# Kernel tuning notes

Measured on AMD Instinct MI355X. Metric: run time of the kernel, lower is better.

The kernel has to match this reference:

```python
import jax, jax.numpy as jnp
import numpy as np

NEG = -1e9

def setup_inputs() -> dict:
    key = jax.random.key(0)
    ks = jax.random.split(key, 8)
    B, Lc, Lq, D = 64, 1024, 128, 128
    C = jax.random.normal(ks[0], (B, Lc, D), dtype=jnp.float32)
    Q = jax.random.normal(ks[1], (B, Lq, D), dtype=jnp.float32)
    Cmask = jax.random.randint(ks[2], (B, Lc), 0, 2, dtype=jnp.int32)
    Qmask = jax.random.randint(ks[3], (B, Lq), 0, 2, dtype=jnp.int32)
    w_c = jax.random.normal(ks[4], (D, 1), dtype=jnp.float32) * (6.0 / (D + 1)) ** 0.5
    w_q = jax.random.normal(ks[5], (D, 1), dtype=jnp.float32) * (6.0 / (D + 1)) ** 0.5
    w_mul = jax.random.normal(ks[6], (1, 1, D), dtype=jnp.float32) * (6.0 / (D + 1)) ** 0.5
    bias = jnp.zeros((1,), dtype=jnp.float32)
    return {"C": C, "Q": Q, "Cmask": Cmask, "Qmask": Qmask,
            "w_c": w_c, "w_q": w_q, "w_mul": w_mul, "bias": bias}

def reference(C, Q, Cmask, Qmask, w_c, w_q, w_mul, bias):
    # Optimized trilinear similarity: S[b,i,j] = C.w_c + Q.w_q + (C*w_mul).Q^T + bias
    s0 = jnp.matmul(C, w_c)                        # [B,Lc,1]
    s1 = jnp.swapaxes(jnp.matmul(Q, w_q), 1, 2)    # [B,1,Lq]
    s2 = jnp.einsum('bid,bjd->bij', C * w_mul, Q)  # [B,Lc,Lq]
    S = s0 + s1 + s2 + bias
    qmask = (Qmask[:, None, :] == 0)               # [B,1,Lq]
    cmask = (Cmask[:, :, None] == 0)               # [B,Lc,1]
    S1 = jax.nn.softmax(jnp.where(qmask, NEG, S), axis=2)
    S2 = jax.nn.softmax(jnp.where(cmask, NEG, S), axis=1)
    A = jnp.matmul(S1, Q)                                       # [B,Lc,D]
    Bm = jnp.matmul(jnp.matmul(S1, jnp.swapaxes(S2, 1, 2)), C)  # [B,Lc,D]
    return jnp.concatenate([C, A, C * A, C * Bm], axis=2)
```

## Files before the change

### kernel.cpp

```cpp
#include <hip/hip_runtime.h>
#include <math.h>

constexpr int Bn = 64, Lc = 1024, Lq = 128, Dd = 128;

typedef __attribute__((ext_vector_type(8))) short short8_t;
typedef __attribute__((ext_vector_type(4))) short short4_t;
typedef __attribute__((ext_vector_type(4))) float f32x4;

__device__ __forceinline__ short f2bf(float x) {
    unsigned u = __float_as_uint(x);
    u += 0x7FFFu + ((u >> 16) & 1u);
    return (short)(u >> 16);
}

constexpr int AS = 132;
constexpr int TS = 70;
constexpr int CTS = 68;
constexpr int PS = 68;
constexpr int TBS = 36;

__device__ __forceinline__ void decode_bid(int n, int& b, int& blk) {
    b = (n & 7) * 8 + ((n >> 3) & 7);
    blk = n >> 6;
}

__global__ __launch_bounds__(256, 3) void k1_fused(
    const float* __restrict__ C, const float* __restrict__ Q,
    const int* __restrict__ Cmask, const int* __restrict__ Qmask,
    const float* __restrict__ w_c, const float* __restrict__ w_q,
    const float* __restrict__ w_mul, const float* __restrict__ bias,
    short* __restrict__ CT16,
    short* __restrict__ Q16, short* __restrict__ QT16,
    float* __restrict__ s0f, float* __restrict__ s1f,
    float* __restrict__ colpart, float* __restrict__ rowsumInv)
{
    __shared__ short Abuf[64 * AS];
    __shared__ short Bbuf[128 * AS];
    __shared__ float s0L[64], cmL[64], s1L[128], qmL[128];
    short* Tbuf = Bbuf;

    int b, blk; decode_bid(blockIdx.x, b, blk);
    int i0 = blk * 64, tid = threadIdx.x;

    const float4* C4 = (const float4*)(C + ((size_t)(b * Lc + i0)) * Dd);
    #pragma unroll
    for (int k = 0; k < 8; ++k) {
        int idx = tid + k * 256;
        int i = idx >> 5, d4 = idx & 31;
        float4 v = C4[idx];
        float4 wm = ((const float4*)w_mul)[d4];
        short4_t cw; cw[0]=f2bf(v.x*wm.x); cw[1]=f2bf(v.y*wm.y); cw[2]=f2bf(v.z*wm.z); cw[3]=f2bf(v.w*wm.w);
        *(short4_t*)&Abuf[i * AS + d4 * 4] = cw;
        float cm = (Cmask[b * Lc + i0 + i] != 0) ? 1.0f : 0.0f;
        Tbuf[(d4*4+0)*TS + i] = f2bf(cm * v.x);
        Tbuf[(d4*4+1)*TS + i] = f2bf(cm * v.y);
        Tbuf[(d4*4+2)*TS + i] = f2bf(cm * v.z);
        Tbuf[(d4*4+3)*TS + i] = f2bf(cm * v.w);
        float4 wc = ((const float4*)w_c)[d4];
        float dot = v.x*wc.x + v.y*wc.y + v.z*wc.z + v.w*wc.w;
        #pragma unroll
        for (int off = 1; off < 32; off <<= 1) dot += __shfl_xor(dot, off, 64);
        if ((tid & 31) == 0) { s0L[i] = dot; cmL[i] = cm; s0f[b * Lc + i0 + i] = dot; }
    }
    __syncthreads();

    #pragma unroll
    for (int k = 0; k < 8; ++k) {
        int idx = tid + k * 256;
        int d = idx >> 4, i4 = idx & 15;
        *(short4_t*)&CT16[((size_t)(b * Dd + d)) * Lc + i0 + i4 * 4] =
            *(short4_t*)&Tbuf[d * TS + i4 * 4];
    }
    __syncthreads();

    const float4* Q4 = (const float4*)(Q + (size_t)b * Lq * Dd);
    #pragma unroll
    for (int k = 0; k < 16; ++k) {
        int idx = tid + k * 256;
        int j = idx >> 5, d4 = idx & 31;
        float4 v = Q4[idx];
        short4_t qv; qv[0]=f2bf(v.x); qv[1]=f2bf(v.y); qv[2]=f2bf(v.z); qv[3]=f2bf(v.w);
        *(short4_t*)&Bbuf[j * AS + d4 * 4] = qv;
        float4 wq = ((const float4*)w_q)[d4];
        float dot = v.x*wq.x + v.y*wq.y + v.z*wq.z + v.w*wq.w;
        #pragma unroll
        for (int off = 1; off < 32; off <<= 1) dot += __shfl_xor(dot, off, 64);
        if ((tid & 31) == 0) {
            s1L[j] = dot;
            qmL[j] = (Qmask[b * Lq + j] != 0) ? 1.0f : 0.0f;
            if (blk == 0) s1f[b * Lq + j] = dot;
        }
    }
    __syncthreads();

    int w = tid >> 6, lane = tid & 63, lm = lane & 15, quad = lane >> 4;
    int iw = i0 + w * 16;
    f32x4 acc[8];
    #pragma unroll
    for (int t = 0; t < 8; ++t) acc[t] = (f32x4){0.f,0.f,0.f,0.f};
    #pragma unroll
    for (int ks = 0; ks < 4; ++ks) {
        short8_t a = *(short8_t*)&Abuf[(w * 16 + lm) * AS + ks * 32 + quad * 8];
        #pragma unroll
        for (int jt = 0; jt < 8; ++jt) {
            short8_t bf = *(short8_t*)&Bbuf[(jt * 16 + lm) * AS + ks * 32 + quad * 8];
            acc[jt] = __builtin_amdgcn_mfma_f32_16x16x32_bf16(a, bf, acc[jt], 0, 0, 0);
        }
    }

    if (blk == 0) {
        #pragma unroll
        for (int k = 0; k < 8; ++k) {
            int idx = tid + k * 256;
            int j = idx >> 4, h = idx & 15;
            *(short8_t*)&Q16[((size_t)(b * Lq + j)) * Dd + h * 8] =
                *(short8_t*)&Bbuf[j * AS + h * 8];
        }
        #pragma unroll
        for (int k = 0; k < 16; ++k) {
            int idx = tid + k * 256;
            int d = idx >> 5, j4 = idx & 31;
            short4_t o;
            #pragma unroll
            for (int r = 0; r < 4; ++r) {
                int j = j4 * 4 + r;
                o[r] = (qmL[j] != 0.f) ? Bbuf[j * AS + d] : (short)0;
            }
            *(short4_t*)&QT16[((size_t)(b * Dd + d)) * Lq + j4 * 4] = o;
        }
    }
    __syncthreads();

    float* colL = (float*)Bbuf;
    float s0v[4], cmv[4];
    #pragma unroll
    for (int r = 0; r < 4; ++r) {
        s0v[r] = s0L[w * 16 + quad * 4 + r];
        cmv[r] = cmL[w * 16 + quad * 4 + r];
    }
    float bb = bias[0];
    float rowpart[4] = {0.f, 0.f, 0.f, 0.f};
    #pragma unroll
    for (int jt = 0; jt < 8; ++jt) {
        int j = jt * 16 + lm;
        float s1 = s1L[j] + bb;
        float qm = qmL[j];
        float cs = 0.f;
        #pragma unroll
        for (int r = 0; r < 4; ++r) {
            float e = __expf(acc[jt][r] + s0v[r] + s1);
            rowpart[r] += qm * e;
            cs += cmv[r] * e;
        }
        cs += __shfl_xor(cs, 16, 64);
        cs += __shfl_xor(cs, 32, 64);
        if (lane < 16) colL[w * 128 + j] = cs;
    }
    #pragma unroll
    for (int r = 0; r < 4; ++r) {
        float v = rowpart[r];
        v += __shfl_xor(v, 1, 64); v += __shfl_xor(v, 2, 64);
        v += __shfl_xor(v, 4, 64); v += __shfl_xor(v, 8, 64);
        if (lm == 0) rowsumInv[b * Lc + iw + quad * 4 + r] = 1.0f / v;
    }
    __syncthreads();
    if (tid < 128)
        colpart[((size_t)b * 16 + blk) * Lq + tid] =
            colL[tid] + colL[128 + tid] + colL[256 + tid] + colL[384 + tid];
}

__global__ __launch_bounds__(512) void k2_T(
    const float* __restrict__ C, const short* __restrict__ CT16,
    const short* __restrict__ Q16, const float* __restrict__ s0f,
    const float* __restrict__ s1f, const float* __restrict__ bias,
    const float* __restrict__ w_mul,
    const int* __restrict__ Qmask, const float* __restrict__ colpart,
    short* __restrict__ TT16)
{
    __shared__ short Qs[32 * AS];
    __shared__ short CWs[64 * AS];
    __shared__ short CTs[128 * CTS];
    __shared__ short Ps[32 * PS];
    __shared__ float s1bL[32], invqL[32], s0L[64];

    int n = blockIdx.x;
    int b, jq; decode_bid(n, b, jq);
    int tid = threadIdx.x, w = tid >> 6, lane = tid & 63;
    int lm = lane & 15, quad = lane >> 4;
    int jh = w & 1, ih = w >> 1;

    {
        int j = tid >> 4, h = tid & 15;
        *(short8_t*)&Qs[j * AS + h * 8] =
            *(const short8_t*)&Q16[((size_t)(b * Lq + jq * 32 + j)) * Dd + h * 8];
    }
    if (tid < 32) {
        int j = jq * 32 + tid;
        s1bL[tid] = s1f[b * Lq + j] + bias[0];
        float cs = 0.f;
        #pragma unroll
        for (int p = 0; p < 16; ++p) cs += colpart[((size_t)b * 16 + p) * Lq + j];
        invqL[tid] = (Qmask[b * Lq + j] != 0) ? 1.0f / cs : 0.0f;
    }

    const float4* Cb4 = (const float4*)(C + (size_t)b * Lc * Dd);
    const short* CTb = CT16 + (size_t)b * Dd * Lc;
    int iS = tid >> 5, dS = tid & 31;
    int dB0 = tid >> 3, dB1 = 64 + (tid >> 3), hB0 = (tid & 7) * 8;
    float4 wmv = ((const float4*)w_mul)[dS];

    float4 pc[4];
    #pragma unroll
    for (int k = 0; k < 4; ++k)
        pc[k] = Cb4[((size_t)(iS + k * 16)) * 32 + dS];
    short8_t wB0 = *(const short8_t*)&CTb[(size_t)dB0 * Lc + hB0];
    short8_t wB1 = *(const short8_t*)&CTb[(size_t)dB1 * Lc + hB0];
    float s0r = (tid < 64) ? s0f[b * Lc + tid] : 0.f;

    f32x4 acc2[2];
    acc2[0] = (f32x4){0.f,0.f,0.f,0.f};
    acc2[1] = (f32x4){0.f,0.f,0.f,0.f};

    for (int ic = 0; ic < 16; ++ic) {
        __syncthreads();
        #pragma unroll
        for (int k = 0; k < 4; ++k) {
            float4 v = pc[k];
            short4_t cw;
            cw[0]=f2bf(v.x*wmv.x); cw[1]=f2bf(v.y*wmv.y); cw[2]=f2bf(v.z*wmv.z); cw[3]=f2bf(v.w*wmv.w);
            *(short4_t*)&CWs[(iS + k * 16) * AS + dS * 4] = cw;
        }
        *(short8_t*)&CTs[dB0 * CTS + hB0] = wB0;
        *(short8_t*)&CTs[dB1 * CTS + hB0] = wB1;
        if (tid < 64) s0L[tid] = s0r;
        if (ic < 15) {
            int ibn = (ic + 1) * 64;
            #pragma unroll
            for (int k = 0; k < 4; ++k)
                pc[k] = Cb4[((size_t)(ibn + iS + k * 16)) * 32 + dS];
            wB0 = *(const short8_t*)&CTb[(size_t)dB0 * Lc + ibn + hB0];
            wB1 = *(const short8_t*)&CTb[(size_t)dB1 * Lc + ibn + hB0];
            if (tid < 64) s0r = s0f[b * Lc + ibn + tid];
        }
        __syncthreads();

        f32x4 sacc = (f32x4){0.f,0.f,0.f,0.f};
        #pragma unroll
        for (int ks = 0; ks < 4; ++ks) {
            short8_t a = *(short8_t*)&Qs[(jh * 16 + lm) * AS + ks * 32 + quad * 8];
            short8_t bf = *(short8_t*)&CWs[(ih * 16 + lm) * AS + ks * 32 + quad * 8];
            sacc = __builtin_amdgcn_mfma_f32_16x16x32_bf16(a, bf, sacc, 0, 0, 0);
        }
        float s0v = s0L[ih * 16 + lm];
        #pragma unroll
        for (int r = 0; r < 4; ++r) {
            float e = __expf(sacc[r] + s0v + s1bL[jh * 16 + quad * 4 + r]);
            Ps[(jh * 16 + quad * 4 + r) * PS + ih * 16 + lm] = f2bf(e);
        }
        __syncthreads();

        #pragma unroll
        for (int ks = 0; ks < 2; ++ks) {
            short8_t a = *(short8_t*)&Ps[(jh * 16 + lm) * PS + ks * 32 + quad * 8];
            #pragma unroll
            for (int t = 0; t < 2; ++t) {
                short8_t bf = *(short8_t*)&CTs[((ih * 2 + t) * 16 + lm) * CTS + ks * 32 + quad * 8];
                acc2[t] = __builtin_amdgcn_mfma_f32_16x16x32_bf16(a, bf, acc2[t], 0, 0, 0);
            }
        }
    }

    short* Tb = CWs;
    #pragma unroll
    for (int t = 0; t < 2; ++t) {
        int d = (ih * 2 + t) * 16 + lm;
        #pragma unroll
        for (int r = 0; r < 4; ++r) {
            int jl = jh * 16 + quad * 4 + r;
            Tb[d * TBS + jl] = f2bf(acc2[t][r] * invqL[jl]);
        }
    }
    __syncthreads();
    #pragma unroll
    for (int k = 0; k < 2; ++k) {
        int idx = tid + k * 512;
        int d = idx >> 3, j4 = idx & 7;
        *(short4_t*)&TT16[((size_t)(b * Dd + d)) * Lq + jq * 32 + j4 * 4] =
            *(short4_t*)&Tb[d * TBS + j4 * 4];
    }
}

__global__ __launch_bounds__(256, 3) void k3_out(
    const short* __restrict__ Q16, const short* __restrict__ QT16,
    const short* __restrict__ TT16, const float* __restrict__ C,
    const float* __restrict__ w_mul, const float* __restrict__ s0f,
    const float* __restrict__ s1f, const float* __restrict__ bias,
    const float* __restrict__ rowsumInv, float* __restrict__ out)
{
    __shared__ short Abuf[64 * AS];
    __shared__ short Bbuf[128 * AS];
    __shared__ float s0L[64], s1bL[128];
    float* Af32 = (float*)Bbuf;

    int n = blockIdx.x;
    int b, blk; decode_bid(n, b, blk);
    int i0 = blk * 64, tid = threadIdx.x;
    int w = tid >> 6, lane = tid & 63, lm = lane & 15, quad = lane >> 4;
    int iw = i0 + w * 16;

    const short8_t* Qg = (const short8_t*)(Q16 + (size_t)b * Lq * Dd);
    #pragma unroll
    for (int k = 0; k < 8; ++k) {
        int idx = tid + k * 256;
        int j = idx >> 4, h = idx & 15;
        *(short8_t*)&Bbuf[j * AS + h * 8] = Qg[idx];
    }
    const float4* C4 = (const float4*)(C + ((size_t)(b * Lc + i0)) * Dd);
    #pragma unroll
    for (int k = 0; k < 8; ++k) {
        int idx = tid + k * 256;
        int i = idx >> 5, d4 = idx & 31;
        float4 v = C4[idx];
        float4 wm = ((const float4*)w_mul)[d4];
        short4_t cw; cw[0]=f2bf(v.x*wm.x); cw[1]=f2bf(v.y*wm.y); cw[2]=f2bf(v.z*wm.z); cw[3]=f2bf(v.w*wm.w);
        *(short4_t*)&Abuf[i * AS + d4 * 4] = cw;
    }
    if (tid < 64) s0L[tid] = s0f[b * Lc + i0 + tid];
    if (tid >= 128 && tid < 256) s1bL[tid - 128] = s1f[b * Lq + tid - 128] + bias[0];
    __syncthreads();

    f32x4 acc[8];
    #pragma unroll
    for (int t = 0; t < 8; ++t) acc[t] = (f32x4){0.f,0.f,0.f,0.f};
    #pragma unroll
    for (int ks = 0; ks < 4; ++ks) {
        short8_t a = *(short8_t*)&Abuf[(w * 16 + lm) * AS + ks * 32 + quad * 8];
        #pragma unroll
        for (int jt = 0; jt < 8; ++jt) {
            short8_t bf = *(short8_t*)&Bbuf[(jt * 16 + lm) * AS + ks * 32 + quad * 8];
            acc[jt] = __builtin_amdgcn_mfma_f32_16x16x32_bf16(a, bf, acc[jt], 0, 0, 0);
        }
    }
    float s0v[4];
    #pragma unroll
    for (int r = 0; r < 4; ++r) s0v[r] = s0L[w * 16 + quad * 4 + r];
    #pragma unroll
    for (int jt = 0; jt < 8; ++jt) {
        int j = jt * 16 + lm;
        float s1b = s1bL[j];
        #pragma unroll
        for (int r = 0; r < 4; ++r) {
            float e = __expf(acc[jt][r] + s0v[r] + s1b);
            Abuf[(w * 16 + quad * 4 + r) * AS + j] = f2bf(e);
        }
    }
    __syncthreads();

    const short8_t* QTg = (const short8_t*)(QT16 + (size_t)b * Dd * Lq);
    #pragma unroll
    for (int k = 0; k < 8; ++k) {
        int idx = tid + k * 256;
        int d = idx >> 4, h = idx & 15;
        *(short8_t*)&Bbuf[d * AS + h * 8] = QTg[idx];
    }
    float rs[4];
    #pragma unroll
    for (int r = 0; r < 4; ++r) rs[r] = rowsumInv[b * Lc + iw + quad * 4 + r];
    __syncthreads();
    f32x4 accQ[8];
    #pragma unroll
    for (int t = 0; t < 8; ++t) accQ[t] = (f32x4){0.f,0.f,0.f,0.f};
    #pragma unroll
    for (int ks = 0; ks < 4; ++ks) {
        short8_t a = *(short8_t*)&Abuf[(w * 16 + lm) * AS + ks * 32 + quad * 8];
        #pragma unroll
        for (int dt = 0; dt < 8; ++dt) {
            short8_t bf = *(short8_t*)&Bbuf[(dt * 16 + lm) * AS + ks * 32 + quad * 8];
            accQ[dt] = __builtin_amdgcn_mfma_f32_16x16x32_bf16(a, bf, accQ[dt], 0, 0, 0);
        }
    }
    __syncthreads();

    #pragma unroll
    for (int dt = 0; dt < 8; ++dt)
        #pragma unroll
        for (int r = 0; r < 4; ++r)
            Af32[(w * 16 + quad * 4 + r) * AS + dt * 16 + lm] = accQ[dt][r] * rs[r];
    __syncthreads();

    #pragma unroll
    for (int k = 0; k < 8; ++k) {
        int idx = tid + k * 256;
        int i = idx >> 5, d4 = idx & 31;
        float4 av = *(float4*)&Af32[i * AS + d4 * 4];
        float4 c = C4[idx];
        size_t base = ((size_t)(b * Lc + i0 + i)) * (4 * Dd) + d4 * 4;
        *(float4*)&out[base]           = c;
        *(float4*)&out[base + Dd]      = av;
        float4 ca; ca.x = c.x*av.x; ca.y = c.y*av.y; ca.z = c.z*av.z; ca.w = c.w*av.w;
        *(float4*)&out[base + 2 * Dd]  = ca;
    }
    __syncthreads();

    const short8_t* TTg = (const short8_t*)(TT16 + (size_t)b * Dd * Lq);
    #pragma unroll
    for (int k = 0; k < 8; ++k) {
        int idx = tid + k * 256;
        int d = idx >> 4, h = idx & 15;
        *(short8_t*)&Bbuf[d * AS + h * 8] = TTg[idx];
    }
    __syncthreads();
    f32x4 accT[8];
    #pragma unroll
    for (int t = 0; t < 8; ++t) accT[t] = (f32x4){0.f,0.f,0.f,0.f};
    #pragma unroll
    for (int ks = 0; ks < 4; ++ks) {
        short8_t a = *(short8_t*)&Abuf[(w * 16 + lm) * AS + ks * 32 + quad * 8];
        #pragma unroll
        for (int dt = 0; dt < 8; ++dt) {
            short8_t bf = *(short8_t*)&Bbuf[(dt * 16 + lm) * AS + ks * 32 + quad * 8];
            accT[dt] = __builtin_amdgcn_mfma_f32_16x16x32_bf16(a, bf, accT[dt], 0, 0, 0);
        }
    }
    __syncthreads();

    #pragma unroll
    for (int dt = 0; dt < 8; ++dt)
        #pragma unroll
        for (int r = 0; r < 4; ++r)
            Af32[(w * 16 + quad * 4 + r) * AS + dt * 16 + lm] = accT[dt][r] * rs[r];
    __syncthreads();

    #pragma unroll
    for (int k = 0; k < 8; ++k) {
        int idx = tid + k * 256;
        int i = idx >> 5, d4 = idx & 31;
        float4 bm = *(float4*)&Af32[i * AS + d4 * 4];
        float4 c = C4[idx];
        size_t base = ((size_t)(b * Lc + i0 + i)) * (4 * Dd) + d4 * 4;
        float4 cb; cb.x = c.x*bm.x; cb.y = c.y*bm.y; cb.z = c.z*bm.z; cb.w = c.w*bm.w;
        *(float4*)&out[base + 3 * Dd]  = cb;
    }
}

extern "C" void kernel_launch(void* const* d_in, const int* in_sizes, int n_in,
                              void* d_out, int out_size, void* d_ws, size_t ws_size,
                              hipStream_t stream) {
    const float* C     = (const float*)d_in[0];
    const float* Q     = (const float*)d_in[1];
    const int*   Cmask = (const int*)d_in[2];
    const int*   Qmask = (const int*)d_in[3];
    const float* w_c   = (const float*)d_in[4];
    const float* w_q   = (const float*)d_in[5];
    const float* w_mul = (const float*)d_in[6];
    const float* bias  = (const float*)d_in[7];
    float* out = (float*)d_out;

    char* p = (char*)d_ws;
    const size_t ND = (size_t)Bn * Lc * Dd;
    const size_t NQ = (size_t)Bn * Lq * Dd;
    short* CT16 = (short*)p; p += ND * 2;
    short* Q16  = (short*)p; p += NQ * 2;
    short* QT16 = (short*)p; p += NQ * 2;
    short* TT16 = (short*)p; p += NQ * 2;
    float* s0f       = (float*)p; p += (size_t)Bn * Lc * 4;
    float* s1f       = (float*)p; p += (size_t)Bn * Lq * 4;
    float* colpart   = (float*)p; p += (size_t)Bn * 16 * Lq * 4;
    float* rowsumInv = (float*)p; p += (size_t)Bn * Lc * 4;

    k1_fused<<<dim3(1024), 256, 0, stream>>>(C, Q, Cmask, Qmask, w_c, w_q, w_mul, bias,
                                             CT16, Q16, QT16, s0f, s1f, colpart, rowsumInv);
    k2_T<<<dim3(256), 512, 0, stream>>>(C, CT16, Q16, s0f, s1f, bias, w_mul, Qmask, colpart, TT16);
    k3_out<<<dim3(1024), 256, 0, stream>>>(Q16, QT16, TT16, C, w_mul, s0f, s1f, bias, rowsumInv, out);
}
```

Baseline: 247.0 us.

## Eliminate first kernel by recomputing column and row softmax sums in consumers

Removes the k1 pass entirely. The T-kernel now converts Q itself, computes s1, the column softmax denominators (accumulated over its own Lc sweep) and writes Q16/QT16. k3 recomputes s0 and the row sums from its own S tile. This drops a launch and the CT16/s0/colpart/rowsumInv round trips through global memory. In exchange the T-kernel must transpose C and reduce with shuffles inside its serial loop over 16 chunks, which could lengthen its critical path on only 256 blocks.

Result: faster. 220.3 us (-10.8%).

```diff
diff --git a/kernel.cpp b/kernel.cpp
--- a/kernel.cpp
+++ b/kernel.cpp
@@ -14,7 +14,6 @@
 }
 
 constexpr int AS = 132;
-constexpr int TS = 70;
 constexpr int CTS = 68;
 constexpr int PS = 68;
 constexpr int TBS = 36;
@@ -24,164 +23,20 @@
     blk = n >> 6;
 }
 
-__global__ __launch_bounds__(256, 3) void k1_fused(
+__global__ __launch_bounds__(512) void kT(
     const float* __restrict__ C, const float* __restrict__ Q,
     const int* __restrict__ Cmask, const int* __restrict__ Qmask,
     const float* __restrict__ w_c, const float* __restrict__ w_q,
     const float* __restrict__ w_mul, const float* __restrict__ bias,
-    short* __restrict__ CT16,
     short* __restrict__ Q16, short* __restrict__ QT16,
-    float* __restrict__ s0f, float* __restrict__ s1f,
-    float* __restrict__ colpart, float* __restrict__ rowsumInv)
-{
-    __shared__ short Abuf[64 * AS];
-    __shared__ short Bbuf[128 * AS];
-    __shared__ float s0L[64], cmL[64], s1L[128], qmL[128];
-    short* Tbuf = Bbuf;
-
-    int b, blk; decode_bid(blockIdx.x, b, blk);
-    int i0 = blk * 64, tid = threadIdx.x;
-
-    const float4* C4 = (const float4*)(C + ((size_t)(b * Lc + i0)) * Dd);
-    #pragma unroll
-    for (int k = 0; k < 8; ++k) {
-        int idx = tid + k * 256;
-        int i = idx >> 5, d4 = idx & 31;
-        float4 v = C4[idx];
-        float4 wm = ((const float4*)w_mul)[d4];
-        short4_t cw; cw[0]=f2bf(v.x*wm.x); cw[1]=f2bf(v.y*wm.y); cw[2]=f2bf(v.z*wm.z); cw[3]=f2bf(v.w*wm.w);
-        *(short4_t*)&Abuf[i * AS + d4 * 4] = cw;
-        float cm = (Cmask[b * Lc + i0 + i] != 0) ? 1.0f : 0.0f;
-        Tbuf[(d4*4+0)*TS + i] = f2bf(cm * v.x);
-        Tbuf[(d4*4+1)*TS + i] = f2bf(cm * v.y);
-        Tbuf[(d4*4+2)*TS + i] = f2bf(cm * v.z);
-        Tbuf[(d4*4+3)*TS + i] = f2bf(cm * v.w);
-        float4 wc = ((const float4*)w_c)[d4];
-        float dot = v.x*wc.x + v.y*wc.y + v.z*wc.z + v.w*wc.w;
-        #pragma unroll
-        for (int off = 1; off < 32; off <<= 1) dot += __shfl_xor(dot, off, 64);
-        if ((tid & 31) == 0) { s0L[i] = dot; cmL[i] = cm; s0f[b * Lc + i0 + i] = dot; }
-    }
-    __syncthreads();
-
-    #pragma unroll
-    for (int k = 0; k < 8; ++k) {
-        int idx = tid + k * 256;
-        int d = idx >> 4, i4 = idx & 15;
-        *(short4_t*)&CT16[((size_t)(b * Dd + d)) * Lc + i0 + i4 * 4] =
-            *(short4_t*)&Tbuf[d * TS + i4 * 4];
-    }
-    __syncthreads();
-
-    const float4* Q4 = (const float4*)(Q + (size_t)b * Lq * Dd);
-    #pragma unroll
-    for (int k = 0; k < 16; ++k) {
-        int idx = tid + k * 256;
-        int j = idx >> 5, d4 = idx & 31;
-        float4 v = Q4[idx];
-        short4_t qv; qv[0]=f2bf(v.x); qv[1]=f2bf(v.y); qv[2]=f2bf(v.z); qv[3]=f2bf(v.w);
-        *(short4_t*)&Bbuf[j * AS + d4 * 4] = qv;
-        float4 wq = ((const float4*)w_q)[d4];
-        float dot = v.x*wq.x + v.y*wq.y + v.z*wq.z + v.w*wq.w;
-        #pragma unroll
-        for (int off = 1; off < 32; off <<= 1) dot += __shfl_xor(dot, off, 64);
-        if ((tid & 31) == 0) {
-            s1L[j] = dot;
-            qmL[j] = (Qmask[b * Lq + j] != 0) ? 1.0f : 0.0f;
-            if (blk == 0) s1f[b * Lq + j] = dot;
-        }
-    }
-    __syncthreads();
-
-    int w = tid >> 6, lane = tid & 63, lm = lane & 15, quad = lane >> 4;
-    int iw = i0 + w * 16;
-    f32x4 acc[8];
-    #pragma unroll
-    for (int t = 0; t < 8; ++t) acc[t] = (f32x4){0.f,0.f,0.f,0.f};
-    #pragma unroll
-    for (int ks = 0; ks < 4; ++ks) {
-        short8_t a = *(short8_t*)&Abuf[(w * 16 + lm) * AS + ks * 32 + quad * 8];
-        #pragma unroll
-        for (int jt = 0; jt < 8; ++jt) {
-            short8_t bf = *(short8_t*)&Bbuf[(jt * 16 + lm) * AS + ks * 32 + quad * 8];
-            acc[jt] = __builtin_amdgcn_mfma_f32_16x16x32_bf16(a, bf, acc[jt], 0, 0, 0);
-        }
-    }
-
-    if (blk == 0) {
-        #pragma unroll
-        for (int k = 0; k < 8; ++k) {
-            int idx = tid + k * 256;
-            int j = idx >> 4, h = idx & 15;
-            *(short8_t*)&Q16[((size_t)(b * Lq + j)) * Dd + h * 8] =
-                *(short8_t*)&Bbuf[j * AS + h * 8];
-        }
-        #pragma unroll
-        for (int k = 0; k < 16; ++k) {
-            int idx = tid + k * 256;
-            int d = idx >> 5, j4 = idx & 31;
-            short4_t o;
-            #pragma unroll
-            for (int r = 0; r < 4; ++r) {
-                int j = j4 * 4 + r;
-                o[r] = (qmL[j] != 0.f) ? Bbuf[j * AS + d] : (short)0;
-            }
-            *(short4_t*)&QT16[((size_t)(b * Dd + d)) * Lq + j4 * 4] = o;
-        }
-    }
-    __syncthreads();
-
-    float* colL = (float*)Bbuf;
-    float s0v[4], cmv[4];
-    #pragma unroll
-    for (int r = 0; r < 4; ++r) {
-        s0v[r] = s0L[w * 16 + quad * 4 + r];
-        cmv[r] = cmL[w * 16 + quad * 4 + r];
-    }
-    float bb = bias[0];
-    float rowpart[4] = {0.f, 0.f, 0.f, 0.f};
-    #pragma unroll
-    for (int jt = 0; jt < 8; ++jt) {
-        int j = jt * 16 + lm;
-        float s1 = s1L[j] + bb;
-        float qm = qmL[j];
-        float cs = 0.f;
-        #pragma unroll
-        for (int r = 0; r < 4; ++r) {
-            float e = __expf(acc[jt][r] + s0v[r] + s1);
-            rowpart[r] += qm * e;
-            cs += cmv[r] * e;
-        }
-        cs += __shfl_xor(cs, 16, 64);
-        cs += __shfl_xor(cs, 32, 64);
-        if (lane < 16) colL[w * 128 + j] = cs;
-    }
-    #pragma unroll
-    for (int r = 0; r < 4; ++r) {
-        float v = rowpart[r];
-        v += __shfl_xor(v, 1, 64); v += __shfl_xor(v, 2, 64);
-        v += __shfl_xor(v, 4, 64); v += __shfl_xor(v, 8, 64);
-        if (lm == 0) rowsumInv[b * Lc + iw + quad * 4 + r] = 1.0f / v;
-    }
-    __syncthreads();
-    if (tid < 128)
-        colpart[((size_t)b * 16 + blk) * Lq + tid] =
-            colL[tid] + colL[128 + tid] + colL[256 + tid] + colL[384 + tid];
-}
-
-__global__ __launch_bounds__(512) void k2_T(
-    const float* __restrict__ C, const short* __restrict__ CT16,
-    const short* __restrict__ Q16, const float* __restrict__ s0f,
-    const float* __restrict__ s1f, const float* __restrict__ bias,
-    const float* __restrict__ w_mul,
-    const int* __restrict__ Qmask, const float* __restrict__ colpart,
-    short* __restrict__ TT16)
+    float* __restrict__ s1f, short* __restrict__ TT16)
 {
     __shared__ short Qs[32 * AS];
     __shared__ short CWs[64 * AS];
     __shared__ short CTs[128 * CTS];
     __shared__ short Ps[32 * PS];
-    __shared__ float s1bL[32], invqL[32], s0L[64];
+    __shared__ float s1bL[32], qmL[32], invqL[32], s0L[64], cmL[64];
+    __shared__ float colAcc[4 * 32];
 
     int n = blockIdx.x;
     int b, jq; decode_bid(n, b, jq);
@@ -190,33 +45,40 @@
     int jh = w & 1, ih = w >> 1;
 
     {
-        int j = tid >> 4, h = tid & 15;
-        *(short8_t*)&Qs[j * AS + h * 8] =
-            *(const short8_t*)&Q16[((size_t)(b * Lq + jq * 32 + j)) * Dd + h * 8];
-    }
-    if (tid < 32) {
-        int j = jq * 32 + tid;
-        s1bL[tid] = s1f[b * Lq + j] + bias[0];
-        float cs = 0.f;
-        #pragma unroll
-        for (int p = 0; p < 16; ++p) cs += colpart[((size_t)b * 16 + p) * Lq + j];
-        invqL[tid] = (Qmask[b * Lq + j] != 0) ? 1.0f / cs : 0.0f;
+        int j = tid >> 4, d4 = tid & 15;
+        const float4* Q4 = (const float4*)(Q + ((size_t)(b * Lq + jq * 32 + j)) * Dd);
+        float4 v0 = Q4[d4], v1 = Q4[d4 + 16];
+        short4_t q0, q1;
+        q0[0]=f2bf(v0.x); q0[1]=f2bf(v0.y); q0[2]=f2bf(v0.z); q0[3]=f2bf(v0.w);
+        q1[0]=f2bf(v1.x); q1[1]=f2bf(v1.y); q1[2]=f2bf(v1.z); q1[3]=f2bf(v1.w);
+        *(short4_t*)&Qs[j * AS + d4 * 4] = q0;
+        *(short4_t*)&Qs[j * AS + (d4 + 16) * 4] = q1;
+        *(short4_t*)&Q16[((size_t)(b * Lq + jq * 32 + j)) * Dd + d4 * 4] = q0;
+        *(short4_t*)&Q16[((size_t)(b * Lq + jq * 32 + j)) * Dd + (d4 + 16) * 4] = q1;
+        float4 wq0 = ((const float4*)w_q)[d4], wq1 = ((const float4*)w_q)[d4 + 16];
+        float dot = v0.x*wq0.x + v0.y*wq0.y + v0.z*wq0.z + v0.w*wq0.w
+                  + v1.x*wq1.x + v1.y*wq1.y + v1.z*wq1.z + v1.w*wq1.w;
+        #pragma unroll
+        for (int off = 1; off < 16; off <<= 1) dot += __shfl_xor(dot, off, 64);
+        if (d4 == 0) {
+            s1bL[j] = dot + bias[0];
+            s1f[b * Lq + jq * 32 + j] = dot;
+            qmL[j] = (Qmask[b * Lq + jq * 32 + j] != 0) ? 1.0f : 0.0f;
+        }
     }
 
     const float4* Cb4 = (const float4*)(C + (size_t)b * Lc * Dd);
-    const short* CTb = CT16 + (size_t)b * Dd * Lc;
     int iS = tid >> 5, dS = tid & 31;
-    int dB0 = tid >> 3, dB1 = 64 + (tid >> 3), hB0 = (tid & 7) * 8;
     float4 wmv = ((const float4*)w_mul)[dS];
-
-    float4 pc[4];
-    #pragma unroll
-    for (int k = 0; k < 4; ++k)
+    float4 wcv = ((const float4*)w_c)[dS];
+    float4 pc[4]; int pm[4];
+    #pragma unroll
+    for (int k = 0; k < 4; ++k) {
         pc[k] = Cb4[((size_t)(iS + k * 16)) * 32 + dS];
-    short8_t wB0 = *(const short8_t*)&CTb[(size_t)dB0 * Lc + hB0];
-    short8_t wB1 = *(const short8_t*)&CTb[(size_t)dB1 * Lc + hB0];
-    float s0r = (tid < 64) ? s0f[b * Lc + tid] : 0.f;
-
+        pm[k] = Cmask[b * Lc + iS + k * 16];
+    }
+
+    float csum[4] = {0.f, 0.f, 0.f, 0.f};
     f32x4 acc2[2];
     acc2[0] = (f32x4){0.f,0.f,0.f,0.f};
     acc2[1] = (f32x4){0.f,0.f,0.f,0.f};
@@ -226,21 +88,27 @@
         #pragma unroll
         for (int k = 0; k < 4; ++k) {
             float4 v = pc[k];
+            float cm = pm[k] ? 1.0f : 0.0f;
+            int i = iS + k * 16;
             short4_t cw;
             cw[0]=f2bf(v.x*wmv.x); cw[1]=f2bf(v.y*wmv.y); cw[2]=f2bf(v.z*wmv.z); cw[3]=f2bf(v.w*wmv.w);
-            *(short4_t*)&CWs[(iS + k * 16) * AS + dS * 4] = cw;
-        }
-        *(short8_t*)&CTs[dB0 * CTS + hB0] = wB0;
-        *(short8_t*)&CTs[dB1 * CTS + hB0] = wB1;
-        if (tid < 64) s0L[tid] = s0r;
+            *(short4_t*)&CWs[i * AS + dS * 4] = cw;
+            CTs[(dS*4+0)*CTS + i] = f2bf(cm * v.x);
+            CTs[(dS*4+1)*CTS + i] = f2bf(cm * v.y);
+            CTs[(dS*4+2)*CTS + i] = f2bf(cm * v.z);
+            CTs[(dS*4+3)*CTS + i] = f2bf(cm * v.w);
+            float dot = v.x*wcv.x + v.y*wcv.y + v.z*wcv.z + v.w*wcv.w;
+            #pragma unroll
+            for (int off = 1; off < 32; off <<= 1) dot += __shfl_xor(dot, off, 64);
+            if (dS == 0) { s0L[i] = dot; cmL[i] = cm; }
+        }
         if (ic < 15) {
             int ibn = (ic + 1) * 64;
             #pragma unroll
-            for (int k = 0; k < 4; ++k)
+            for (int k = 0; k < 4; ++k) {
                 pc[k] = Cb4[((size_t)(ibn + iS + k * 16)) * 32 + dS];
-            wB0 = *(const short8_t*)&CTb[(size_t)dB0 * Lc + ibn + hB0];
-            wB1 = *(const short8_t*)&CTb[(size_t)dB1 * Lc + ibn + hB0];
-            if (tid < 64) s0r = s0f[b * Lc + ibn + tid];
+                pm[k] = Cmask[b * Lc + ibn + iS + k * 16];
+            }
         }
         __syncthreads();
 
@@ -248,14 +116,16 @@
         #pragma unroll
         for (int ks = 0; ks < 4; ++ks) {
             short8_t a = *(short8_t*)&Qs[(jh * 16 + lm) * AS + ks * 32 + quad * 8];
-            short8_t bf = *(short8_t*)&CWs[(ih * 16 + lm) * AS + ks * 32 + quad * 8];
-            sacc = __builtin_amdgcn_mfma_f32_16x16x32_bf16(a, bf, sacc, 0, 0, 0);
+            short8_t bq = *(short8_t*)&CWs[(ih * 16 + lm) * AS + ks * 32 + quad * 8];
+            sacc = __builtin_amdgcn_mfma_f32_16x16x32_bf16(a, bq, sacc, 0, 0, 0);
         }
         float s0v = s0L[ih * 16 + lm];
+        float cmv = cmL[ih * 16 + lm];
         #pragma unroll
         for (int r = 0; r < 4; ++r) {
             float e = __expf(sacc[r] + s0v + s1bL[jh * 16 + quad * 4 + r]);
             Ps[(jh * 16 + quad * 4 + r) * PS + ih * 16 + lm] = f2bf(e);
+            csum[r] += cmv * e;
         }
         __syncthreads();
 
@@ -270,6 +140,20 @@
         }
     }
 
+    #pragma unroll
+    for (int r = 0; r < 4; ++r) {
+        float v = csum[r];
+        v += __shfl_xor(v, 1, 64); v += __shfl_xor(v, 2, 64);
+        v += __shfl_xor(v, 4, 64); v += __shfl_xor(v, 8, 64);
+        if (lm == 0) colAcc[ih * 32 + jh * 16 + quad * 4 + r] = v;
+    }
+    __syncthreads();
+    if (tid < 32) {
+        float cs = colAcc[tid] + colAcc[32 + tid] + colAcc[64 + tid] + colAcc[96 + tid];
+        invqL[tid] = (qmL[tid] != 0.f) ? 1.0f / cs : 0.0f;
+    }
+    __syncthreads();
+
     short* Tb = CWs;
     #pragma unroll
     for (int t = 0; t < 2; ++t) {
@@ -288,25 +172,36 @@
         *(short4_t*)&TT16[((size_t)(b * Dd + d)) * Lq + jq * 32 + j4 * 4] =
             *(short4_t*)&Tb[d * TBS + j4 * 4];
     }
+
+    {
+        int d = tid >> 2, j8 = (tid & 3) * 8;
+        short8_t o;
+        #pragma unroll
+        for (int r = 0; r < 8; ++r) {
+            int j = j8 + r;
+            o[r] = (qmL[j] != 0.f) ? Qs[j * AS + d] : (short)0;
+        }
+        *(short8_t*)&QT16[((size_t)(b * Dd + d)) * Lq + jq * 32 + j8] = o;
+    }
 }
 
 __global__ __launch_bounds__(256, 3) void k3_out(
     const short* __restrict__ Q16, const short* __restrict__ QT16,
     const short* __restrict__ TT16, const float* __restrict__ C,
-    const float* __restrict__ w_mul, const float* __restrict__ s0f,
+    const float* __restrict__ w_mul, const float* __restrict__ w_c,
+    const int* __restrict__ Qmask,
     const float* __restrict__ s1f, const float* __restrict__ bias,
-    const float* __restrict__ rowsumInv, float* __restrict__ out)
+    float* __restrict__ out)
 {
     __shared__ short Abuf[64 * AS];
     __shared__ short Bbuf[128 * AS];
-    __shared__ float s0L[64], s1bL[128];
+    __shared__ float s0L[64], s1bL[128], qmLf[128];
     float* Af32 = (float*)Bbuf;
 
     int n = blockIdx.x;
     int b, blk; decode_bid(n, b, blk);
     int i0 = blk * 64, tid = threadIdx.x;
     int w = tid >> 6, lane = tid & 63, lm = lane & 15, quad = lane >> 4;
-    int iw = i0 + w * 16;
 
     const short8_t* Qg = (const short8_t*)(Q16 + (size_t)b * Lq * Dd);
     #pragma unroll
@@ -324,9 +219,16 @@
         float4 wm = ((const float4*)w_mul)[d4];
         short4_t cw; cw[0]=f2bf(v.x*wm.x); cw[1]=f2bf(v.y*wm.y); cw[2]=f2bf(v.z*wm.z); cw[3]=f2bf(v.w*wm.w);
         *(short4_t*)&Abuf[i * AS + d4 * 4] = cw;
-    }
-    if (tid < 64) s0L[tid] = s0f[b * Lc + i0 + tid];
-    if (tid >= 128 && tid < 256) s1bL[tid - 128] = s1f[b * Lq + tid - 128] + bias[0];
+        float4 wc = ((const float4*)w_c)[d4];
+        float dot = v.x*wc.x + v.y*wc.y + v.z*wc.z + v.w*wc.w;
+        #pragma unroll
+        for (int off = 1; off < 32; off <<= 1) dot += __shfl_xor(dot, off, 64);
+        if ((tid & 31) == 0) s0L[i] = dot;
+    }
+    if (tid < 128) {
+        s1bL[tid] = s1f[b * Lq + tid] + bias[0];
+        qmLf[tid] = (Qmask[b * Lq + tid] != 0) ? 1.0f : 0.0f;
+    }
     __syncthreads();
 
     f32x4 acc[8];
@@ -341,18 +243,30 @@
             acc[jt] = __builtin_amdgcn_mfma_f32_16x16x32_bf16(a, bf, acc[jt], 0, 0, 0);
         }
     }
+
     float s0v[4];
     #pragma unroll
     for (int r = 0; r < 4; ++r) s0v[r] = s0L[w * 16 + quad * 4 + r];
+    float rowpart[4] = {0.f, 0.f, 0.f, 0.f};
     #pragma unroll
     for (int jt = 0; jt < 8; ++jt) {
         int j = jt * 16 + lm;
         float s1b = s1bL[j];
+        float qm = qmLf[j];
         #pragma unroll
         for (int r = 0; r < 4; ++r) {
             float e = __expf(acc[jt][r] + s0v[r] + s1b);
             Abuf[(w * 16 + quad * 4 + r) * AS + j] = f2bf(e);
-        }
+            rowpart[r] += qm * e;
+        }
+    }
+    float rs[4];
+    #pragma unroll
+    for (int r = 0; r < 4; ++r) {
+        float v = rowpart[r];
+        v += __shfl_xor(v, 1, 64); v += __shfl_xor(v, 2, 64);
+        v += __shfl_xor(v, 4, 64); v += __shfl_xor(v, 8, 64);
+        rs[r] = 1.0f / v;
     }
     __syncthreads();
 
@@ -363,9 +277,6 @@
         int d = idx >> 4, h = idx & 15;
         *(short8_t*)&Bbuf[d * AS + h * 8] = QTg[idx];
     }
-    float rs[4];
-    #pragma unroll
-    for (int r = 0; r < 4; ++r) rs[r] = rowsumInv[b * Lc + iw + quad * 4 + r];
     __syncthreads();
     f32x4 accQ[8];
     #pragma unroll
@@ -457,19 +368,14 @@
     float* out = (float*)d_out;
 
     char* p = (char*)d_ws;
-    const size_t ND = (size_t)Bn * Lc * Dd;
     const size_t NQ = (size_t)Bn * Lq * Dd;
-    short* CT16 = (short*)p; p += ND * 2;
     short* Q16  = (short*)p; p += NQ * 2;
     short* QT16 = (short*)p; p += NQ * 2;
     short* TT16 = (short*)p; p += NQ * 2;
-    float* s0f       = (float*)p; p += (size_t)Bn * Lc * 4;
-    float* s1f       = (float*)p; p += (size_t)Bn * Lq * 4;
-    float* colpart   = (float*)p; p += (size_t)Bn * 16 * Lq * 4;
-    float* rowsumInv = (float*)p; p += (size_t)Bn * Lc * 4;
-
-    k1_fused<<<dim3(1024), 256, 0, stream>>>(C, Q, Cmask, Qmask, w_c, w_q, w_mul, bias,
-                                             CT16, Q16, QT16, s0f, s1f, colpart, rowsumInv);
-    k2_T<<<dim3(256), 512, 0, stream>>>(C, CT16, Q16, s0f, s1f, bias, w_mul, Qmask, colpart, TT16);
-    k3_out<<<dim3(1024), 256, 0, stream>>>(Q16, QT16, TT16, C, w_mul, s0f, s1f, bias, rowsumInv, out);
-}
+    float* s1f  = (float*)p; p += (size_t)Bn * Lq * 4;
+
+    kT<<<dim3(256), 512, 0, stream>>>(C, Q, Cmask, Qmask, w_c, w_q, w_mul, bias,
+                                      Q16, QT16, s1f, TT16);
+    k3_out<<<dim3(1024), 256, 0, stream>>>(Q16, QT16, TT16, C, w_mul, w_c, Qmask,
+                                           s1f, bias, out);
+}
```
